# Kernel tuning notes

Hardware: AMD Instinct MI355X
Metric: run time of the kernel (lower is better)

Reference implementation:

```python
import jax, jax.numpy as jnp
import numpy as np

TGT, SRC, BATCH, HID, ATT = 64, 64, 32, 512, 512

def setup_inputs() -> dict:
    key = jax.random.key(0)
    k1, k2, k3, k4 = jax.random.split(key, 4)
    h_t = jax.random.normal(k1, (TGT, BATCH, HID), dtype=jnp.float32)
    src_encodings = jax.random.normal(k2, (SRC, BATCH, HID), dtype=jnp.float32)
    # Wa: Linear(2*HID -> ATT, bias=False); stored as (in, out) for jnp.
    Wa = jax.random.normal(k3, (2 * HID, ATT), dtype=jnp.float32) * (1.0 / np.sqrt(2 * HID))
    # Va: Linear(ATT -> 1, bias=False)
    Va = jax.random.normal(k4, (ATT,), dtype=jnp.float32) * (1.0 / np.sqrt(ATT))
    return {"h_t": h_t, "src_encodings": src_encodings, "Wa": Wa, "Va": Va}

def reference(h_t, src_encodings, Wa, Va):
    # Wa([h_t, src]) = h_t @ Wa_h + src @ Wa_s (exact by linearity of concat-matmul)
    Wa_h, Wa_s = Wa[:HID], Wa[HID:]                 # (H, A) each
    h_part = jnp.einsum('tbh,ha->tba', h_t, Wa_h)   # (T, B, A)
    s_part = jnp.einsum('sbh,ha->sba', src_encodings, Wa_s)  # (S, B, A)
    # scores[s, t, b] = Va . tanh(h_part[t,b] + s_part[s,b])
    hidden = jnp.tanh(h_part[None, :, :, :] + s_part[:, None, :, :])  # (S, T, B, A)
    scores = jnp.einsum('stba,a->stb', hidden, Va)  # (S, T, B)
    attn = jax.nn.softmax(scores, axis=0)           # softmax over src dim
    # context[t,b,:] = sum_s attn[s,t,b] * src[s,b,:]
    context = jnp.einsum('stb,sbh->tbh', attn, src_encodings)  # (T, B, H)
    return context
```

## Files before the change

kernel.cpp:

```cpp
#include <hip/hip_runtime.h>
#include <hip/hip_bf16.h>

#define TGT   64
#define SRCN  64
#define BATCH 32
#define HID   512
#define ATT   512
#define MROWS (TGT * BATCH)

typedef __bf16 bf16_t;
typedef __bf16 bf16x8 __attribute__((ext_vector_type(8)));
typedef float  f32x4  __attribute__((ext_vector_type(4)));

__device__ __forceinline__ float fast_exp2(float x) {
#if __has_builtin(__builtin_amdgcn_exp2f)
  return __builtin_amdgcn_exp2f(x);
#else
  float r; asm("v_exp_f32 %0, %1\n\ts_nop 1" : "=v"(r) : "v"(x)); return r;
#endif
}
__device__ __forceinline__ float fast_rcp(float x) {
#if __has_builtin(__builtin_amdgcn_rcpf)
  return __builtin_amdgcn_rcpf(x);
#else
  float r; asm("v_rcp_f32 %0, %1\n\ts_nop 1" : "=v"(r) : "v"(x)); return r;
#endif
}

#define MFMA(a, b, c) __builtin_amdgcn_mfma_f32_16x16x32_bf16((a), (b), (c), 0, 0, 0)

#define SC_EXP 2.8853900817779268f

__global__ __launch_bounds__(256) void proj_gemm(
    const float* __restrict__ h_t, const float* __restrict__ srcp,
    const float* __restrict__ Wa, float* __restrict__ C)
{
  const int z = blockIdx.z;
  const float* __restrict__ A = z ? srcp : h_t;
  const int mbase = blockIdx.x * 64;
  const int nbase = blockIdx.y * 64;

  __shared__ bf16_t Ah[64][72];
  __shared__ bf16_t Al[64][72];
  __shared__ bf16_t Bh[64][72];
  __shared__ bf16_t Bl[64][72];

  const int tid  = threadIdx.x;
  const int lane = tid & 63;
  const int wv   = tid >> 6;
  const int wm   = (wv & 1) * 32;
  const int wn   = (wv >> 1) * 32;
  const int l15  = lane & 15;
  const int qd   = lane >> 4;

  const int arow = tid >> 2;
  const int akc  = (tid & 3) * 16;
  const int bn = tid & 63;
  const int bkg = (tid >> 6) * 16;

  const float* Aptr = A + (size_t)(mbase + arow) * HID + akc;
  const float* Bptr = Wa + (size_t)(z * HID + bkg) * ATT + nbase + bn;

  f32x4 acc00 = {0.f, 0.f, 0.f, 0.f};
  f32x4 acc01 = acc00, acc10 = acc00, acc11 = acc00;

  float4 pa0 = *(const float4*)(Aptr);
  float4 pa1 = *(const float4*)(Aptr + 4);
  float4 pa2 = *(const float4*)(Aptr + 8);
  float4 pa3 = *(const float4*)(Aptr + 12);
  float pb[16];
#pragma unroll
  for (int j = 0; j < 16; ++j) pb[j] = Bptr[(size_t)j * ATT];

  for (int kb = 0; kb < HID; kb += 64) {
    if (kb) __syncthreads();

    {
      float av[16] = {pa0.x, pa0.y, pa0.z, pa0.w, pa1.x, pa1.y, pa1.z, pa1.w,
                      pa2.x, pa2.y, pa2.z, pa2.w, pa3.x, pa3.y, pa3.z, pa3.w};
      bf16x8 hi0, hi1, lo0, lo1;
#pragma unroll
      for (int j = 0; j < 8; ++j) {
        bf16_t h = (bf16_t)av[j];
        hi0[j] = h;
        lo0[j] = (bf16_t)(av[j] - (float)h);
        bf16_t h2 = (bf16_t)av[j + 8];
        hi1[j] = h2;
        lo1[j] = (bf16_t)(av[j + 8] - (float)h2);
      }
      *(bf16x8*)&Ah[arow][akc]     = hi0;
      *(bf16x8*)&Ah[arow][akc + 8] = hi1;
      *(bf16x8*)&Al[arow][akc]     = lo0;
      *(bf16x8*)&Al[arow][akc + 8] = lo1;
    }

    {
      bf16x8 hi0, hi1, lo0, lo1;
#pragma unroll
      for (int j = 0; j < 8; ++j) {
        bf16_t h = (bf16_t)pb[j];
        hi0[j] = h;
        lo0[j] = (bf16_t)(pb[j] - (float)h);
        bf16_t h2 = (bf16_t)pb[j + 8];
        hi1[j] = h2;
        lo1[j] = (bf16_t)(pb[j + 8] - (float)h2);
      }
      *(bf16x8*)&Bh[bn][bkg]     = hi0;
      *(bf16x8*)&Bh[bn][bkg + 8] = hi1;
      *(bf16x8*)&Bl[bn][bkg]     = lo0;
      *(bf16x8*)&Bl[bn][bkg + 8] = lo1;
    }
    __syncthreads();

    const int kn = kb + 64;
    if (kn < HID) {
      pa0 = *(const float4*)(Aptr + kn);
      pa1 = *(const float4*)(Aptr + kn + 4);
      pa2 = *(const float4*)(Aptr + kn + 8);
      pa3 = *(const float4*)(Aptr + kn + 12);
      const float* bp = Bptr + (size_t)kn * ATT;
#pragma unroll
      for (int j = 0; j < 16; ++j) pb[j] = bp[(size_t)j * ATT];
    }

#pragma unroll
    for (int h = 0; h < 2; ++h) {
      const int kh = h * 32 + qd * 8;
      bf16x8 ah0 = *(const bf16x8*)&Ah[wm + l15][kh];
      bf16x8 ah1 = *(const bf16x8*)&Ah[wm + 16 + l15][kh];
      bf16x8 al0 = *(const bf16x8*)&Al[wm + l15][kh];
      bf16x8 al1 = *(const bf16x8*)&Al[wm + 16 + l15][kh];
      bf16x8 bh0 = *(const bf16x8*)&Bh[wn + l15][kh];
      bf16x8 bh1 = *(const bf16x8*)&Bh[wn + 16 + l15][kh];
      bf16x8 bl0 = *(const bf16x8*)&Bl[wn + l15][kh];
      bf16x8 bl1 = *(const bf16x8*)&Bl[wn + 16 + l15][kh];

      acc00 = MFMA(ah0, bh0, acc00);
      acc01 = MFMA(ah0, bh1, acc01);
      acc10 = MFMA(ah1, bh0, acc10);
      acc11 = MFMA(ah1, bh1, acc11);
      acc00 = MFMA(al0, bh0, acc00);
      acc01 = MFMA(al0, bh1, acc01);
      acc10 = MFMA(al1, bh0, acc10);
      acc11 = MFMA(al1, bh1, acc11);
      acc00 = MFMA(ah0, bl0, acc00);
      acc01 = MFMA(ah0, bl1, acc01);
      acc10 = MFMA(ah1, bl0, acc10);
      acc11 = MFMA(ah1, bl1, acc11);
    }
  }

  float* Cz = C + (size_t)z * (MROWS * ATT);
#pragma unroll
  for (int r = 0; r < 4; ++r) {
    int row0 = mbase + wm + qd * 4 + r;
    int row1 = row0 + 16;
    int col0 = nbase + wn + l15;
    Cz[(size_t)row0 * ATT + col0]      = fast_exp2(acc00[r] * SC_EXP);
    Cz[(size_t)row0 * ATT + col0 + 16] = fast_exp2(acc01[r] * SC_EXP);
    Cz[(size_t)row1 * ATT + col0]      = fast_exp2(acc10[r] * SC_EXP);
    Cz[(size_t)row1 * ATT + col0 + 16] = fast_exp2(acc11[r] * SC_EXP);
  }
}

__global__ __launch_bounds__(512) void attn_fused(
    const float* __restrict__ ws, const float* __restrict__ srcp,
    const float* __restrict__ Va, float* __restrict__ out)
{
  const float* __restrict__ eh_part = ws;
  const float* __restrict__ es_part = ws + (size_t)TGT * BATCH * ATT;

  const int t0   = blockIdx.x * 4;
  const int b    = blockIdx.y;
  const int tid  = threadIdx.x;
  const int lane = tid & 63;
  const int wv   = tid >> 6;

  __shared__ float scoreLds[4][64];
  __shared__ float attnLds[4][64];

  const int abase = lane * 8;
  float va[8], eH[4][8];
  *(float4*)&va[0] = *(const float4*)(Va + abase);
  *(float4*)&va[4] = *(const float4*)(Va + abase + 4);

  float vsum = 0.f;
#pragma unroll
  for (int j = 0; j < 8; ++j) vsum += va[j];
#pragma unroll
  for (int off = 32; off; off >>= 1) vsum += __shfl_xor(vsum, off);

#pragma unroll
  for (int t = 0; t < 4; ++t) {
    const float* hp = eh_part + ((size_t)(t0 + t) * BATCH + b) * ATT + abase;
    *(float4*)&eH[t][0] = *(const float4*)hp;
    *(float4*)&eH[t][4] = *(const float4*)(hp + 4);
  }

  const bool hi32 = (lane & 32) != 0;
  const bool hi16 = (lane & 16) != 0;

#pragma unroll 2
  for (int i = 0; i < 8; ++i) {
    const int s = wv * 8 + i;
    const float* sp = es_part + ((size_t)s * BATCH + b) * ATT + abase;
    float ex[8];
    *(float4*)&ex[0] = *(const float4*)sp;
    *(float4*)&ex[4] = *(const float4*)(sp + 4);

    float q0 = 0.f, q1 = 0.f, q2 = 0.f, q3 = 0.f;
#pragma unroll
    for (int j = 0; j < 8; ++j) {
      float e = ex[j];
      float vj = va[j];
      float y0 = fmaf(e, eH[0][j], 1.0f);
      float y1 = fmaf(e, eH[1][j], 1.0f);
      float y2 = fmaf(e, eH[2][j], 1.0f);
      float y3 = fmaf(e, eH[3][j], 1.0f);
      float r01 = fast_rcp(y0 * y1);
      float r23 = fast_rcp(y2 * y3);
      q0 = fmaf(vj * y1, r01, q0);
      q1 = fmaf(vj * y0, r01, q1);
      q2 = fmaf(vj * y3, r23, q2);
      q3 = fmaf(vj * y2, r23, q3);
    }

    float a02 = hi32 ? q2 : q0;
    float b02 = hi32 ? q0 : q2;
    float a13 = hi32 ? q3 : q1;
    float b13 = hi32 ? q1 : q3;
    a02 += __shfl_xor(b02, 32);
    a13 += __shfl_xor(b13, 32);
    float x = hi16 ? a13 : a02;
    float y = hi16 ? a02 : a13;
    x += __shfl_xor(y, 16);
    x += __shfl_xor(x, 8);
    x += __shfl_xor(x, 4);
    x += __shfl_xor(x, 2);
    x += __shfl_xor(x, 1);
    if ((lane & 15) == 0) scoreLds[lane >> 4][s] = vsum - 2.0f * x;
  }
  __syncthreads();

  if (wv < 4) {
    float sc = scoreLds[wv][lane];
    float m = sc;
#pragma unroll
    for (int off = 32; off; off >>= 1) m = fmaxf(m, __shfl_xor(m, off));
    float e = fast_exp2((sc - m) * 1.4426950408889634f);
    float ssum = e;
#pragma unroll
    for (int off = 32; off; off >>= 1) ssum += __shfl_xor(ssum, off);
    attnLds[wv][lane] = e * fast_rcp(ssum);
  }
  __syncthreads();

  {
    float c0 = 0.f, c1 = 0.f, c2 = 0.f, c3 = 0.f;
    const float* sb = srcp + (size_t)b * HID + tid;
#pragma unroll 8
    for (int s = 0; s < SRCN; ++s) {
      float sv = sb[(size_t)s * BATCH * HID];
      c0 = fmaf(attnLds[0][s], sv, c0);
      c1 = fmaf(attnLds[1][s], sv, c1);
      c2 = fmaf(attnLds[2][s], sv, c2);
      c3 = fmaf(attnLds[3][s], sv, c3);
    }
    out[((size_t)(t0 + 0) * BATCH + b) * HID + tid] = c0;
    out[((size_t)(t0 + 1) * BATCH + b) * HID + tid] = c1;
    out[((size_t)(t0 + 2) * BATCH + b) * HID + tid] = c2;
    out[((size_t)(t0 + 3) * BATCH + b) * HID + tid] = c3;
  }
}

extern "C" void kernel_launch(void* const* d_in, const int* in_sizes, int n_in,
                              void* d_out, int out_size, void* d_ws, size_t ws_size,
                              hipStream_t stream) {
  const float* h_t = (const float*)d_in[0];
  const float* src = (const float*)d_in[1];
  const float* Wa  = (const float*)d_in[2];
  const float* Va  = (const float*)d_in[3];
  float* out = (float*)d_out;
  float* C   = (float*)d_ws;

  proj_gemm<<<dim3(32, 8, 2), 256, 0, stream>>>(h_t, src, Wa, C);
  attn_fused<<<dim3(16, 32), 512, 0, stream>>>(C, src, Va, out);
}
```

Baseline: 95.44 us.

## Double-buffer GEMM LDS tiles and process eight targets per attention block

The projection GEMM now alternates between two LDS buffers, which removes the barrier at the top of each k-iteration. The attention kernel now handles eight target positions per block instead of four. This reuses each loaded source projection row and the src values across twice as many targets, and the grid is halved to 256 blocks. In exchange it uses more registers and gives fewer blocks across the CUs.

```diff
diff --git a/kernel.cpp b/kernel.cpp
--- a/kernel.cpp
+++ b/kernel.cpp
@@ -40,10 +40,10 @@
   const int mbase = blockIdx.x * 64;
   const int nbase = blockIdx.y * 64;
 
-  __shared__ bf16_t Ah[64][72];
-  __shared__ bf16_t Al[64][72];
-  __shared__ bf16_t Bh[64][72];
-  __shared__ bf16_t Bl[64][72];
+  __shared__ bf16_t Ah[2][64][72];
+  __shared__ bf16_t Al[2][64][72];
+  __shared__ bf16_t Bh[2][64][72];
+  __shared__ bf16_t Bl[2][64][72];
 
   const int tid  = threadIdx.x;
   const int lane = tid & 63;
@@ -72,8 +72,9 @@
 #pragma unroll
   for (int j = 0; j < 16; ++j) pb[j] = Bptr[(size_t)j * ATT];
 
-  for (int kb = 0; kb < HID; kb += 64) {
-    if (kb) __syncthreads();
+#pragma unroll 1
+  for (int it = 0; it < 8; ++it) {
+    const int buf = it & 1;
 
     {
       float av[16] = {pa0.x, pa0.y, pa0.z, pa0.w, pa1.x, pa1.y, pa1.z, pa1.w,
@@ -88,10 +89,10 @@
         hi1[j] = h2;
         lo1[j] = (bf16_t)(av[j + 8] - (float)h2);
       }
-      *(bf16x8*)&Ah[arow][akc]     = hi0;
-      *(bf16x8*)&Ah[arow][akc + 8] = hi1;
-      *(bf16x8*)&Al[arow][akc]     = lo0;
-      *(bf16x8*)&Al[arow][akc + 8] = lo1;
+      *(bf16x8*)&Ah[buf][arow][akc]     = hi0;
+      *(bf16x8*)&Ah[buf][arow][akc + 8] = hi1;
+      *(bf16x8*)&Al[buf][arow][akc]     = lo0;
+      *(bf16x8*)&Al[buf][arow][akc + 8] = lo1;
     }
 
     {
@@ -105,14 +106,14 @@
         hi1[j] = h2;
         lo1[j] = (bf16_t)(pb[j + 8] - (float)h2);
       }
-      *(bf16x8*)&Bh[bn][bkg]     = hi0;
-      *(bf16x8*)&Bh[bn][bkg + 8] = hi1;
-      *(bf16x8*)&Bl[bn][bkg]     = lo0;
-      *(bf16x8*)&Bl[bn][bkg + 8] = lo1;
+      *(bf16x8*)&Bh[buf][bn][bkg]     = hi0;
+      *(bf16x8*)&Bh[buf][bn][bkg + 8] = hi1;
+      *(bf16x8*)&Bl[buf][bn][bkg]     = lo0;
+      *(bf16x8*)&Bl[buf][bn][bkg + 8] = lo1;
     }
     __syncthreads();
 
-    const int kn = kb + 64;
+    const int kn = (it + 1) * 64;
     if (kn < HID) {
       pa0 = *(const float4*)(Aptr + kn);
       pa1 = *(const float4*)(Aptr + kn + 4);
@@ -126,14 +127,14 @@
 #pragma unroll
     for (int h = 0; h < 2; ++h) {
       const int kh = h * 32 + qd * 8;
-      bf16x8 ah0 = *(const bf16x8*)&Ah[wm + l15][kh];
-      bf16x8 ah1 = *(const bf16x8*)&Ah[wm + 16 + l15][kh];
-      bf16x8 al0 = *(const bf16x8*)&Al[wm + l15][kh];
-      bf16x8 al1 = *(const bf16x8*)&Al[wm + 16 + l15][kh];
-      bf16x8 bh0 = *(const bf16x8*)&Bh[wn + l15][kh];
-      bf16x8 bh1 = *(const bf16x8*)&Bh[wn + 16 + l15][kh];
-      bf16x8 bl0 = *(const bf16x8*)&Bl[wn + l15][kh];
-      bf16x8 bl1 = *(const bf16x8*)&Bl[wn + 16 + l15][kh];
+      bf16x8 ah0 = *(const bf16x8*)&Ah[buf][wm + l15][kh];
+      bf16x8 ah1 = *(const bf16x8*)&Ah[buf][wm + 16 + l15][kh];
+      bf16x8 al0 = *(const bf16x8*)&Al[buf][wm + l15][kh];
+      bf16x8 al1 = *(const bf16x8*)&Al[buf][wm + 16 + l15][kh];
+      bf16x8 bh0 = *(const bf16x8*)&Bh[buf][wn + l15][kh];
+      bf16x8 bh1 = *(const bf16x8*)&Bh[buf][wn + 16 + l15][kh];
+      bf16x8 bl0 = *(const bf16x8*)&Bl[buf][wn + l15][kh];
+      bf16x8 bl1 = *(const bf16x8*)&Bl[buf][wn + 16 + l15][kh];
 
       acc00 = MFMA(ah0, bh0, acc00);
       acc01 = MFMA(ah0, bh1, acc01);
@@ -170,17 +171,17 @@
   const float* __restrict__ eh_part = ws;
   const float* __restrict__ es_part = ws + (size_t)TGT * BATCH * ATT;
 
-  const int t0   = blockIdx.x * 4;
+  const int t0   = blockIdx.x * 8;
   const int b    = blockIdx.y;
   const int tid  = threadIdx.x;
   const int lane = tid & 63;
   const int wv   = tid >> 6;
 
-  __shared__ float scoreLds[4][64];
-  __shared__ float attnLds[4][64];
+  __shared__ float scoreLds[8][64];
+  __shared__ float attnLds[8][64];
 
   const int abase = lane * 8;
-  float va[8], eH[4][8];
+  float va[8], eH[8][8];
   *(float4*)&va[0] = *(const float4*)(Va + abase);
   *(float4*)&va[4] = *(const float4*)(Va + abase + 4);
 
@@ -191,7 +192,7 @@
   for (int off = 32; off; off >>= 1) vsum += __shfl_xor(vsum, off);
 
 #pragma unroll
-  for (int t = 0; t < 4; ++t) {
+  for (int t = 0; t < 8; ++t) {
     const float* hp = eh_part + ((size_t)(t0 + t) * BATCH + b) * ATT + abase;
     *(float4*)&eH[t][0] = *(const float4*)hp;
     *(float4*)&eH[t][4] = *(const float4*)(hp + 4);
@@ -199,6 +200,7 @@
 
   const bool hi32 = (lane & 32) != 0;
   const bool hi16 = (lane & 16) != 0;
+  const bool hi8  = (lane & 8)  != 0;
 
 #pragma unroll 2
   for (int i = 0; i < 8; ++i) {
@@ -209,6 +211,7 @@
     *(float4*)&ex[4] = *(const float4*)(sp + 4);
 
     float q0 = 0.f, q1 = 0.f, q2 = 0.f, q3 = 0.f;
+    float q4 = 0.f, q5 = 0.f, q6 = 0.f, q7 = 0.f;
 #pragma unroll
     for (int j = 0; j < 8; ++j) {
       float e = ex[j];
@@ -217,32 +220,46 @@
       float y1 = fmaf(e, eH[1][j], 1.0f);
       float y2 = fmaf(e, eH[2][j], 1.0f);
       float y3 = fmaf(e, eH[3][j], 1.0f);
+      float y4 = fmaf(e, eH[4][j], 1.0f);
+      float y5 = fmaf(e, eH[5][j], 1.0f);
+      float y6 = fmaf(e, eH[6][j], 1.0f);
+      float y7 = fmaf(e, eH[7][j], 1.0f);
       float r01 = fast_rcp(y0 * y1);
       float r23 = fast_rcp(y2 * y3);
+      float r45 = fast_rcp(y4 * y5);
+      float r67 = fast_rcp(y6 * y7);
       q0 = fmaf(vj * y1, r01, q0);
       q1 = fmaf(vj * y0, r01, q1);
       q2 = fmaf(vj * y3, r23, q2);
       q3 = fmaf(vj * y2, r23, q3);
-    }
-
-    float a02 = hi32 ? q2 : q0;
-    float b02 = hi32 ? q0 : q2;
-    float a13 = hi32 ? q3 : q1;
-    float b13 = hi32 ? q1 : q3;
-    a02 += __shfl_xor(b02, 32);
-    a13 += __shfl_xor(b13, 32);
-    float x = hi16 ? a13 : a02;
-    float y = hi16 ? a02 : a13;
-    x += __shfl_xor(y, 16);
-    x += __shfl_xor(x, 8);
+      q4 = fmaf(vj * y5, r45, q4);
+      q5 = fmaf(vj * y4, r45, q5);
+      q6 = fmaf(vj * y7, r67, q6);
+      q7 = fmaf(vj * y6, r67, q7);
+    }
+
+    float a0 = hi32 ? q4 : q0, b0 = hi32 ? q0 : q4;
+    float a1 = hi32 ? q5 : q1, b1 = hi32 ? q1 : q5;
+    float a2 = hi32 ? q6 : q2, b2 = hi32 ? q2 : q6;
+    float a3 = hi32 ? q7 : q3, b3 = hi32 ? q3 : q7;
+    a0 += __shfl_xor(b0, 32);
+    a1 += __shfl_xor(b1, 32);
+    a2 += __shfl_xor(b2, 32);
+    a3 += __shfl_xor(b3, 32);
+    float c0 = hi16 ? a2 : a0, d0 = hi16 ? a0 : a2;
+    float c1 = hi16 ? a3 : a1, d1 = hi16 ? a1 : a3;
+    c0 += __shfl_xor(d0, 16);
+    c1 += __shfl_xor(d1, 16);
+    float x = hi8 ? c1 : c0, y = hi8 ? c0 : c1;
+    x += __shfl_xor(y, 8);
     x += __shfl_xor(x, 4);
     x += __shfl_xor(x, 2);
     x += __shfl_xor(x, 1);
-    if ((lane & 15) == 0) scoreLds[lane >> 4][s] = vsum - 2.0f * x;
+    if ((lane & 7) == 0) scoreLds[lane >> 3][s] = vsum - 2.0f * x;
   }
   __syncthreads();
 
-  if (wv < 4) {
+  {
     float sc = scoreLds[wv][lane];
     float m = sc;
 #pragma unroll
@@ -257,6 +274,7 @@
 
   {
     float c0 = 0.f, c1 = 0.f, c2 = 0.f, c3 = 0.f;
+    float c4 = 0.f, c5 = 0.f, c6 = 0.f, c7 = 0.f;
     const float* sb = srcp + (size_t)b * HID + tid;
 #pragma unroll 8
     for (int s = 0; s < SRCN; ++s) {
@@ -265,11 +283,19 @@
       c1 = fmaf(attnLds[1][s], sv, c1);
       c2 = fmaf(attnLds[2][s], sv, c2);
       c3 = fmaf(attnLds[3][s], sv, c3);
+      c4 = fmaf(attnLds[4][s], sv, c4);
+      c5 = fmaf(attnLds[5][s], sv, c5);
+      c6 = fmaf(attnLds[6][s], sv, c6);
+      c7 = fmaf(attnLds[7][s], sv, c7);
     }
     out[((size_t)(t0 + 0) * BATCH + b) * HID + tid] = c0;
     out[((size_t)(t0 + 1) * BATCH + b) * HID + tid] = c1;
     out[((size_t)(t0 + 2) * BATCH + b) * HID + tid] = c2;
     out[((size_t)(t0 + 3) * BATCH + b) * HID + tid] = c3;
+    out[((size_t)(t0 + 4) * BATCH + b) * HID + tid] = c4;
+    out[((size_t)(t0 + 5) * BATCH + b) * HID + tid] = c5;
+    out[((size_t)(t0 + 6) * BATCH + b) * HID + tid] = c6;
+    out[((size_t)(t0 + 7) * BATCH + b) * HID + tid] = c7;
   }
 }
 
@@ -284,5 +310,5 @@
   float* C   = (float*)d_ws;
 
   proj_gemm<<<dim3(32, 8, 2), 256, 0, stream>>>(h_t, src, Wa, C);
-  attn_fused<<<dim3(16, 32), 512, 0, stream>>>(C, src, Va, out);
-}
+  attn_fused<<<dim3(8, 32), 512, 0, stream>>>(C, src, Va, out);
+}
```

Measured after the change: 96.66 us. About the same (+1.3%).
